# Performance work log

Hardware: AMD Instinct MI355X
Metric: run time of the kernel (lower is better)

Reference implementation:

```python
import jax, jax.numpy as jnp
import numpy as np

B, T, I, H, O = 32, 2048, 512, 512, 256


def setup_inputs() -> dict:
    key = jax.random.key(0)
    ks = jax.random.split(key, 11)
    s_in = 1.0 / np.sqrt(I)  # torch Linear default init bound
    s_h = 1.0 / np.sqrt(H)

    def lin(k, shape, s):
        return jax.random.uniform(k, shape, jnp.float32, -s, s)

    return {
        "x": jax.random.normal(ks[0], (B, T, I), jnp.float32),
        "W_i": lin(ks[1], (H, I), s_in), "b_i": lin(ks[2], (H,), s_in),
        "W_f": lin(ks[3], (H, I), s_in), "b_f": lin(ks[4], (H,), s_in),
        "W_g": lin(ks[5], (H, I), s_in), "b_g": lin(ks[6], (H,), s_in),
        "W_o": lin(ks[7], (H, I), s_in), "b_o": lin(ks[8], (H,), s_in),
        "W_fc": lin(ks[9], (O, H), s_h), "b_fc": lin(ks[10], (O,), s_h),
    }


def reference(x, W_i, b_i, W_f, b_f, W_g, b_g, W_o, b_o, W_fc, b_fc):
    # NOTE: this module's gates depend on x only (not h), so all four gate
    # projections can be precomputed as one pass of GEMMs over [B,T,I].
    gi = jax.nn.sigmoid(jnp.einsum("bti,hi->bth", x, W_i) + b_i)
    gf = jax.nn.sigmoid(jnp.einsum("bti,hi->bth", x, W_f) + b_f)
    gg = jnp.tanh(jnp.einsum("bti,hi->bth", x, W_g) + b_g)
    go = jax.nn.sigmoid(jnp.einsum("bti,hi->bth", x, W_o) + b_o)

    # Sequential elementwise recurrence over time (time-major for scan).
    def step(carry, gates_t):
        _, c = carry
        i, f, g, o = gates_t
        c = f * c + i * g
        h = o * jnp.tanh(c)
        return (h, c), None

    init = (jnp.zeros((B, H), x.dtype), jnp.zeros((B, H), x.dtype))
    gates_tm = (gi.swapaxes(0, 1), gf.swapaxes(0, 1),
                gg.swapaxes(0, 1), go.swapaxes(0, 1))  # each [T,B,H]
    (h, _), _ = jax.lax.scan(step, init, gates_tm)

    return h @ W_fc.T + b_fc  # [B, O]
```

## Files before the change

kernel.cpp:

```cpp
#include <hip/hip_runtime.h>
#include <stdint.h>

#define DI 512
#define DH 512
#define DOUT 256
#define NB 32
#define NT 2048
#define MTOT (NB*NT)
#define NCHUNK 16
#define CLEN 128
#define BM 128
#define BN 64
#define BK 32

typedef unsigned short u16;
typedef __attribute__((ext_vector_type(8))) short bf16x8;
typedef __attribute__((ext_vector_type(4))) short s16x4;
typedef __attribute__((ext_vector_type(4))) float f32x4;

__device__ __forceinline__ u16 f2bf(float f) {
    union { float f; unsigned int u; } c; c.f = f;
    unsigned int u = c.u;
    u += 0x7fffu + ((u >> 16) & 1u);
    return (u16)(u >> 16);
}
__device__ __forceinline__ float bf2f(u16 h) {
    union { unsigned int u; float f; } c; c.u = ((unsigned int)h) << 16;
    return c.f;
}
__device__ __forceinline__ float sigm(float x) { return 1.0f / (1.0f + __expf(-x)); }
__device__ __forceinline__ float tanh_(float x) { return 1.0f - 2.0f / (__expf(2.0f * x) + 1.0f); }

__global__ __launch_bounds__(256)
void cvt_all(const float* __restrict__ X, const float* __restrict__ w0,
             const float* __restrict__ w1, const float* __restrict__ w2,
             u16* __restrict__ xbf, u16* __restrict__ wbf) {
    const int NX4 = MTOT * DI / 4;
    const int NW4 = DH * DI / 4;
    const int total = NX4 + 3 * NW4;
    const int stride = gridDim.x * blockDim.x;
    for (int i = blockIdx.x * blockDim.x + threadIdx.x; i < total; i += stride) {
        const float4* s4; ushort4* d4; int j;
        if (i < NX4) {
            s4 = reinterpret_cast<const float4*>(X);
            d4 = reinterpret_cast<ushort4*>(xbf);
            j = i;
        } else {
            const int k = i - NX4;
            const int w = k >> 16;
            j = k & 65535;
            s4 = reinterpret_cast<const float4*>(w == 0 ? w0 : w == 1 ? w1 : w2);
            d4 = reinterpret_cast<ushort4*>(wbf + (size_t)w * DH * DI);
        }
        float4 v = s4[j];
        unsigned int lo, hi;
        asm("v_cvt_pk_bf16_f32 %0, %1, %2" : "=v"(lo) : "v"(v.x), "v"(v.y));
        asm("v_cvt_pk_bf16_f32 %0, %1, %2" : "=v"(hi) : "v"(v.z), "v"(v.w));
        ushort4 o;
        o.x = (u16)(lo & 0xffffu); o.y = (u16)(lo >> 16);
        o.z = (u16)(hi & 0xffffu); o.w = (u16)(hi >> 16);
        d4[j] = o;
    }
}

__global__ __launch_bounds__(256, 3)
void gate_gemm_scan(const u16* __restrict__ Xbf, const u16* __restrict__ W,
                    const float* __restrict__ b_i, const float* __restrict__ b_f,
                    const float* __restrict__ b_g,
                    float* __restrict__ Ach, float* __restrict__ Vch) {
    __shared__ __align__(16) union {
        struct { u16 sA[2][BM * BK]; u16 sB[2][3 * BN * BK]; } st;
        struct { u16 Ft[BN][132]; u16 Pt[BN][132]; float pa[256]; float pv[256]; } sc;
    } u;

    const int bid0 = blockIdx.x;
    const int swz = (bid0 & 7) * 512 + (bid0 >> 3);
    const int mtile = swz >> 3;
    const int ntile = swz & 7;
    const int m0 = mtile * BM;
    const int n0 = ntile * BN;

    const int tid = threadIdx.x;
    const int lane = tid & 63;
    const int ws = __builtin_amdgcn_readfirstlane(tid >> 6);
    const int wr = ws >> 1;
    const int wc = ws & 1;

    const int srow = lane >> 2;
    const int slot = lane & 3;
    const int fr = lane & 15;
    const int khalf = lane >> 4;

    const int rlA = ws * 32 + srow;
    const int swzslot = slot ^ ((rlA >> 1) & 3);
    const u16* pA0 = Xbf + (size_t)(m0 + rlA) * DI + swzslot * 8;
    const u16* pA1 = pA0 + (size_t)16 * DI;

    const int idx0 = ws * 3;
    const int g0 = idx0 >> 2, cc0 = idx0 & 3;
    const int rlB0 = cc0 * 16 + srow;
    const u16* gaB0 = W + (size_t)g0 * DH * DI + (size_t)(n0 + rlB0) * DI
                    + ((slot ^ ((rlB0 >> 1) & 3)) * 8);
    int dB[3];
    dB[0] = 0;
#pragma unroll
    for (int q = 1; q < 3; ++q) {
        const int idxq = idx0 + q;
        const int gq = idxq >> 2, ccq = idxq & 3;
        dB[q] = __builtin_amdgcn_readfirstlane((gq - g0) * (DH * DI) + (ccq - cc0) * 16 * DI);
    }

    const int rA = wr * 64 + fr;
    const int offA0 = rA * BK + ((khalf ^ ((rA >> 1) & 3)) * 8);
    const int rB = wc * 32 + fr;
    const int offB0 = rB * BK + ((khalf ^ ((rB >> 1) & 3)) * 8);

#define STAGE_A(CB, KT) do {                                                        \
    u16* sAb = u.st.sA[(CB)];                                                       \
    __builtin_amdgcn_global_load_lds(                                               \
        (const __attribute__((address_space(1))) unsigned int*)(pA0 + (KT) * BK),   \
        (__attribute__((address_space(3))) unsigned int*)(sAb + (ws * 2 + 0) * 512),\
        16, 0, 0);                                                                  \
    __builtin_amdgcn_global_load_lds(                                               \
        (const __attribute__((address_space(1))) unsigned int*)(pA1 + (KT) * BK),   \
        (__attribute__((address_space(3))) unsigned int*)(sAb + (ws * 2 + 1) * 512),\
        16, 0, 0);                                                                  \
} while (0)

#define STAGE_B(CB, KT) do {                                                        \
    u16* sBb = u.st.sB[(CB)];                                                       \
    _Pragma("unroll")                                                               \
    for (int q = 0; q < 3; ++q) {                                                   \
        const int idxq = ws * 3 + q;                                                \
        __builtin_amdgcn_global_load_lds(                                           \
            (const __attribute__((address_space(1))) unsigned int*)(gaB0 + dB[q] + (KT) * BK), \
            (__attribute__((address_space(3))) unsigned int*)(sBb + (idxq >> 2) * (BN * BK) + (idxq & 3) * 512), \
            16, 0, 0);                                                              \
    }                                                                               \
} while (0)

    f32x4 acc[3][4][2] = {};

    STAGE_A(0, 0);
    STAGE_B(0, 0);

#define KSTEP(KT) do {                                                              \
    constexpr int cur_ = (KT) & 1;                                                  \
    constexpr int nxt_ = cur_ ^ 1;                                                  \
    if ((KT) < 15) {                                                                \
        STAGE_A(nxt_, (KT) + 1);                                                    \
        STAGE_B(nxt_, (KT) + 1);                                                    \
        asm volatile("s_waitcnt vmcnt(5)" ::: "memory");                            \
    } else {                                                                        \
        asm volatile("s_waitcnt vmcnt(0)" ::: "memory");                            \
    }                                                                               \
    __builtin_amdgcn_sched_barrier(0);                                              \
    __builtin_amdgcn_s_barrier();                                                   \
    {                                                                               \
        const u16* sAb = u.st.sA[cur_];                                             \
        const u16* sBb = u.st.sB[cur_];                                             \
        bf16x8 af[4];                                                               \
        _Pragma("unroll")                                                           \
        for (int m = 0; m < 4; m++)                                                 \
            af[m] = *reinterpret_cast<const bf16x8*>(sAb + offA0 + m * 16 * BK);    \
        __builtin_amdgcn_s_setprio(1);                                              \
        _Pragma("unroll")                                                           \
        for (int g = 0; g < 3; g++) {                                               \
            const u16* sbg = sBb + g * (BN * BK);                                   \
            bf16x8 b0 = *reinterpret_cast<const bf16x8*>(sbg + offB0);              \
            bf16x8 b1 = *reinterpret_cast<const bf16x8*>(sbg + offB0 + 16 * BK);    \
            _Pragma("unroll")                                                       \
            for (int m = 0; m < 4; m++) {                                           \
                acc[g][m][0] = __builtin_amdgcn_mfma_f32_16x16x32_bf16(af[m], b0, acc[g][m][0], 0, 0, 0); \
                acc[g][m][1] = __builtin_amdgcn_mfma_f32_16x16x32_bf16(af[m], b1, acc[g][m][1], 0, 0, 0); \
            }                                                                       \
        }                                                                           \
        __builtin_amdgcn_s_setprio(0);                                              \
    }                                                                               \
    if ((KT) < 15) {                                                                \
        __builtin_amdgcn_sched_barrier(0);                                          \
        __builtin_amdgcn_s_barrier();                                               \
    }                                                                               \
} while (0)

    KSTEP(0);  KSTEP(1);  KSTEP(2);  KSTEP(3);
    KSTEP(4);  KSTEP(5);  KSTEP(6);  KSTEP(7);
    KSTEP(8);  KSTEP(9);  KSTEP(10); KSTEP(11);
    KSTEP(12); KSTEP(13); KSTEP(14); KSTEP(15);
#undef KSTEP
#undef STAGE_B
#undef STAGE_A

    __syncthreads();

    const int rbase = (lane >> 4) * 4;
#pragma unroll
    for (int n = 0; n < 2; n++) {
        const int cl = wc * 32 + n * 16 + fr;
        const int hg = n0 + cl;
        const float bi_ = b_i[hg];
        const float bfv = b_f[hg];
        const float bg_ = b_g[hg];
#pragma unroll
        for (int m = 0; m < 4; m++) {
            const int rr0 = wr * 64 + m * 16 + rbase;
            s16x4 fpk, ppk;
#pragma unroll
            for (int jj = 0; jj < 4; jj++) {
                const float fi = sigm(acc[0][m][n][jj] + bi_);
                const float ff = sigm(acc[1][m][n][jj] + bfv);
                const float fg = tanh_(acc[2][m][n][jj] + bg_);
                fpk[jj] = (short)f2bf(ff);
                ppk[jj] = (short)f2bf(fi * fg);
            }
            *reinterpret_cast<s16x4*>(&u.sc.Ft[cl][rr0]) = fpk;
            *reinterpret_cast<s16x4*>(&u.sc.Pt[cl][rr0]) = ppk;
        }
    }
    __syncthreads();

    {
        const int h = tid & 63;
        const int q = tid >> 6;
        const int t0 = q * 32;
        float a = 1.0f, v = 0.0f;
#pragma unroll
        for (int kk = 0; kk < 8; kk++) {
            s16x4 fv = *reinterpret_cast<const s16x4*>(&u.sc.Ft[h][t0 + kk * 4]);
            s16x4 pv4 = *reinterpret_cast<const s16x4*>(&u.sc.Pt[h][t0 + kk * 4]);
#pragma unroll
            for (int e = 0; e < 4; e++) {
                const float f = bf2f((u16)fv[e]);
                const float p = bf2f((u16)pv4[e]);
                v = f * v + p;
                a *= f;
            }
        }
        u.sc.pa[tid] = a;
        u.sc.pv[tid] = v;
    }
    __syncthreads();

    if (tid < 64) {
        float Aacc = u.sc.pa[tid];
        float Vacc = u.sc.pv[tid];
#pragma unroll
        for (int q = 1; q < 4; q++) {
            const float aq = u.sc.pa[q * 64 + tid];
            const float vq = u.sc.pv[q * 64 + tid];
            Vacc = aq * Vacc + vq;
            Aacc *= aq;
        }
        const size_t o = (size_t)mtile * DH + n0 + tid;
        Ach[o] = Aacc;
        Vch[o] = Vacc;
    }
}

__global__ void cvt_w3(const float* __restrict__ w0, const float* __restrict__ w1,
                       const float* __restrict__ w2, u16* __restrict__ out) {
    const int per = DH * DI / 4;
    int gid = blockIdx.x * blockDim.x + threadIdx.x;
    int wsel = gid / per;
    int i = gid - wsel * per;
    const float* src = (wsel == 0) ? w0 : (wsel == 1) ? w1 : w2;
    float4 v = reinterpret_cast<const float4*>(src)[i];
    ushort4 o;
    o.x = f2bf(v.x); o.y = f2bf(v.y); o.z = f2bf(v.z); o.w = f2bf(v.w);
    reinterpret_cast<ushort4*>(out + (size_t)wsel * DH * DI)[i] = o;
}

__global__ __launch_bounds__(256, 2)
void gate_gemm_scan_fused(const float* __restrict__ X, const u16* __restrict__ W,
                          const float* __restrict__ b_i, const float* __restrict__ b_f,
                          const float* __restrict__ b_g,
                          float* __restrict__ Ach, float* __restrict__ Vch) {
    __shared__ __align__(16) union {
        struct { u16 sA[2][BM * BK]; u16 sB[2][3 * BN * BK]; } st;
        struct { u16 Ft[BN][132]; u16 Pt[BN][132]; float pa[256]; float pv[256]; } sc;
    } u;

    const int bid0 = blockIdx.x;
    const int swz = (bid0 & 7) * 512 + (bid0 >> 3);
    const int mtile = swz >> 3;
    const int ntile = swz & 7;
    const int m0 = mtile * BM;
    const int n0 = ntile * BN;

    const int tid = threadIdx.x;
    const int lane = tid & 63;
    const int ws = __builtin_amdgcn_readfirstlane(tid >> 6);
    const int wr = ws >> 1;
    const int wc = ws & 1;

    const int srow = lane >> 2;
    const int slot = lane & 3;
    const int fr = lane & 15;
    const int khalf = lane >> 4;

    const int rlA = ws * 32 + srow;
    const int swzslot = slot ^ ((rlA >> 1) & 3);
    const float* pXA = X + (size_t)(m0 + rlA) * DI + swzslot * 8;

    const int idx0 = ws * 3;
    const int g0 = idx0 >> 2, cc0 = idx0 & 3;
    const int rlB0 = cc0 * 16 + srow;
    const u16* gaB0 = W + (size_t)g0 * DH * DI + (size_t)(n0 + rlB0) * DI
                    + ((slot ^ ((rlB0 >> 1) & 3)) * 8);
    int dB[3];
    dB[0] = 0;
#pragma unroll
    for (int q = 1; q < 3; ++q) {
        const int idxq = idx0 + q;
        const int gq = idxq >> 2, ccq = idxq & 3;
        dB[q] = __builtin_amdgcn_readfirstlane((gq - g0) * (DH * DI) + (ccq - cc0) * 16 * DI);
    }

    const int rA = wr * 64 + fr;
    const int offA0 = rA * BK + ((khalf ^ ((rA >> 1) & 3)) * 8);
    const int rB = wc * 32 + fr;
    const int offB0 = rB * BK + ((khalf ^ ((rB >> 1) & 3)) * 8);

    float4 fa[2][2][2];

#define LOAD_A(P, KT) do {                                                          \
    _Pragma("unroll")                                                               \
    for (int s = 0; s < 2; ++s) {                                                   \
        fa[(P)][s][0] = *reinterpret_cast<const float4*>(pXA + (size_t)s * 16 * DI + (KT) * 32);     \
        fa[(P)][s][1] = *reinterpret_cast<const float4*>(pXA + (size_t)s * 16 * DI + (KT) * 32 + 4); \
    }                                                                               \
} while (0)

#define CVT_STAGE(P, CB) do {                                                       \
    _Pragma("unroll")                                                               \
    for (int s = 0; s < 2; ++s) {                                                   \
        unsigned int pk0, pk1, pk2, pk3;                                            \
        asm("v_cvt_pk_bf16_f32 %0, %1, %2" : "=v"(pk0) : "v"(fa[(P)][s][0].x), "v"(fa[(P)][s][0].y)); \
        asm("v_cvt_pk_bf16_f32 %0, %1, %2" : "=v"(pk1) : "v"(fa[(P)][s][0].z), "v"(fa[(P)][s][0].w)); \
        asm("v_cvt_pk_bf16_f32 %0, %1, %2" : "=v"(pk2) : "v"(fa[(P)][s][1].x), "v"(fa[(P)][s][1].y)); \
        asm("v_cvt_pk_bf16_f32 %0, %1, %2" : "=v"(pk3) : "v"(fa[(P)][s][1].z), "v"(fa[(P)][s][1].w)); \
        uint4 wv; wv.x = pk0; wv.y = pk1; wv.z = pk2; wv.w = pk3;                   \
        *reinterpret_cast<uint4*>(u.st.sA[(CB)] + ((ws * 2 + s) * 512 + lane * 8)) = wv; \
    }                                                                               \
} while (0)

#define STAGE_B(CB, KT) do {                                                        \
    u16* sBb = u.st.sB[(CB)];                                                       \
    _Pragma("unroll")                                                               \
    for (int q = 0; q < 3; ++q) {                                                   \
        const int idxq = ws * 3 + q;                                                \
        __builtin_amdgcn_global_load_lds(                                           \
            (const __attribute__((address_space(1))) unsigned int*)(gaB0 + dB[q] + (KT) * BK), \
            (__attribute__((address_space(3))) unsigned int*)(sBb + (idxq >> 2) * (BN * BK) + (idxq & 3) * 512), \
            16, 0, 0);                                                              \
    }                                                                               \
} while (0)

    f32x4 acc[3][4][2] = {};

    LOAD_A(0, 0);
    LOAD_A(1, 1);
    CVT_STAGE(0, 0);
    STAGE_B(0, 0);
    asm volatile("s_waitcnt vmcnt(0)" ::: "memory");
    asm volatile("s_waitcnt lgkmcnt(0)" ::: "memory");
    __builtin_amdgcn_sched_barrier(0);
    __builtin_amdgcn_s_barrier();

#define KSTEP(KT) do {                                                              \
    constexpr int cur_ = (KT) & 1;                                                  \
    constexpr int nxt_ = cur_ ^ 1;                                                  \
    if ((KT) < 15) {                                                                \
        CVT_STAGE(nxt_, nxt_);                                                      \
        STAGE_B(nxt_, (KT) + 1);                                                    \
    }                                                                               \
    if ((KT) < 14) LOAD_A(cur_, (KT) + 2);                                          \
    if ((KT) == 15) asm volatile("s_waitcnt vmcnt(0)" ::: "memory");                \
    __builtin_amdgcn_sched_barrier(0);                                              \
    __builtin_amdgcn_s_barrier();                                                   \
    {                                                                               \
        const u16* sAb = u.st.sA[cur_];                                             \
        const u16* sBb = u.st.sB[cur_];                                             \
        bf16x8 af[4];                                                               \
        _Pragma("unroll")                                                           \
        for (int m = 0; m < 4; m++)                                                 \
            af[m] = *reinterpret_cast<const bf16x8*>(sAb + offA0 + m * 16 * BK);    \
        __builtin_amdgcn_s_setprio(1);                                              \
        _Pragma("unroll")                                                           \
        for (int g = 0; g < 3; g++) {                                               \
            const u16* sbg = sBb + g * (BN * BK);                                   \
            bf16x8 b0 = *reinterpret_cast<const bf16x8*>(sbg + offB0);              \
            bf16x8 b1 = *reinterpret_cast<const bf16x8*>(sbg + offB0 + 16 * BK);    \
            _Pragma("unroll")                                                       \
            for (int m = 0; m < 4; m++) {                                           \
                acc[g][m][0] = __builtin_amdgcn_mfma_f32_16x16x32_bf16(af[m], b0, acc[g][m][0], 0, 0, 0); \
                acc[g][m][1] = __builtin_amdgcn_mfma_f32_16x16x32_bf16(af[m], b1, acc[g][m][1], 0, 0, 0); \
            }                                                                       \
        }                                                                           \
        __builtin_amdgcn_s_setprio(0);                                              \
    }                                                                               \
    if ((KT) < 15) {                                                                \
        asm volatile("s_waitcnt lgkmcnt(0)" ::: "memory");                          \
        __builtin_amdgcn_sched_barrier(0);                                          \
        __builtin_amdgcn_s_barrier();                                               \
    }                                                                               \
} while (0)

    KSTEP(0);  KSTEP(1);  KSTEP(2);  KSTEP(3);
    KSTEP(4);  KSTEP(5);  KSTEP(6);  KSTEP(7);
    KSTEP(8);  KSTEP(9);  KSTEP(10); KSTEP(11);
    KSTEP(12); KSTEP(13); KSTEP(14); KSTEP(15);
#undef KSTEP
#undef STAGE_B
#undef CVT_STAGE
#undef LOAD_A

    __syncthreads();

    const int rbase = (lane >> 4) * 4;
#pragma unroll
    for (int n = 0; n < 2; n++) {
        const int cl = wc * 32 + n * 16 + fr;
        const int hg = n0 + cl;
        const float bi_ = b_i[hg];
        const float bfv = b_f[hg];
        const float bg_ = b_g[hg];
#pragma unroll
        for (int m = 0; m < 4; m++) {
            const int rr0 = wr * 64 + m * 16 + rbase;
            s16x4 fpk, ppk;
#pragma unroll
            for (int jj = 0; jj < 4; jj++) {
                const float fi = sigm(acc[0][m][n][jj] + bi_);
                const float ff = sigm(acc[1][m][n][jj] + bfv);
                const float fg = tanh_(acc[2][m][n][jj] + bg_);
                fpk[jj] = (short)f2bf(ff);
                ppk[jj] = (short)f2bf(fi * fg);
            }
            *reinterpret_cast<s16x4*>(&u.sc.Ft[cl][rr0]) = fpk;
            *reinterpret_cast<s16x4*>(&u.sc.Pt[cl][rr0]) = ppk;
        }
    }
    __syncthreads();

    {
        const int h = tid & 63;
        const int q = tid >> 6;
        const int t0 = q * 32;
        float a = 1.0f, v = 0.0f;
#pragma unroll
        for (int kk = 0; kk < 8; kk++) {
            s16x4 fv = *reinterpret_cast<const s16x4*>(&u.sc.Ft[h][t0 + kk * 4]);
            s16x4 pv4 = *reinterpret_cast<const s16x4*>(&u.sc.Pt[h][t0 + kk * 4]);
#pragma unroll
            for (int e = 0; e < 4; e++) {
                const float f = bf2f((u16)fv[e]);
                const float p = bf2f((u16)pv4[e]);
                v = f * v + p;
                a *= f;
            }
        }
        u.sc.pa[tid] = a;
        u.sc.pv[tid] = v;
    }
    __syncthreads();

    if (tid < 64) {
        float Aacc = u.sc.pa[tid];
        float Vacc = u.sc.pv[tid];
#pragma unroll
        for (int q = 1; q < 4; q++) {
            const float aq = u.sc.pa[q * 64 + tid];
            const float vq = u.sc.pv[q * 64 + tid];
            Vacc = aq * Vacc + vq;
            Aacc *= aq;
        }
        const size_t o = (size_t)mtile * DH + n0 + tid;
        Ach[o] = Aacc;
        Vch[o] = Vacc;
    }
}

__global__ __launch_bounds__(512)
void finalize_fc(const float* __restrict__ Ach, const float* __restrict__ Vch,
                 const float* __restrict__ x, const float* __restrict__ Wo,
                 const float* __restrict__ bo, const float* __restrict__ Wfc,
                 const float* __restrict__ bfc, float* __restrict__ out) {
    __shared__ float xrow[DI];
    __shared__ float hrow[DH];
    const int b = blockIdx.x;
    const int tid = threadIdx.x;

    xrow[tid] = x[((size_t)b * NT + (NT - 1)) * DI + tid];
    float c = 0.0f;
#pragma unroll
    for (int jj = 0; jj < NCHUNK; jj++) {
        const size_t o = ((size_t)(b * NCHUNK + jj)) * DH + tid;
        c = Ach[o] * c + Vch[o];
    }
    __syncthreads();

    {
        const float4* xr = reinterpret_cast<const float4*>(xrow);
        const float4* wrow = reinterpret_cast<const float4*>(Wo + (size_t)tid * DI);
        float dot = 0.0f;
#pragma unroll 4
        for (int k = 0; k < DI / 4; k++) {
            float4 xv = xr[k];
            float4 wv = wrow[k];
            dot += xv.x * wv.x + xv.y * wv.y + xv.z * wv.z + xv.w * wv.w;
        }
        const float og = sigm(dot + bo[tid]);
        hrow[tid] = og * tanh_(c);
    }
    __syncthreads();

    if (tid < DOUT) {
        const float4* hr = reinterpret_cast<const float4*>(hrow);
        const float4* wrow = reinterpret_cast<const float4*>(Wfc + (size_t)tid * DH);
        float acc = 0.0f;
#pragma unroll 4
        for (int k = 0; k < DH / 4; k++) {
            float4 hv = hr[k];
            float4 wv = wrow[k];
            acc += hv.x * wv.x + hv.y * wv.y + hv.z * wv.z + hv.w * wv.w;
        }
        out[b * DOUT + tid] = acc + bfc[tid];
    }
}

extern "C" void kernel_launch(void* const* d_in, const int* in_sizes, int n_in,
                              void* d_out, int out_size, void* d_ws, size_t ws_size,
                              hipStream_t stream) {
    const float* x    = (const float*)d_in[0];
    const float* W_i  = (const float*)d_in[1];
    const float* b_i  = (const float*)d_in[2];
    const float* W_f  = (const float*)d_in[3];
    const float* b_f  = (const float*)d_in[4];
    const float* W_g  = (const float*)d_in[5];
    const float* b_g  = (const float*)d_in[6];
    const float* W_o  = (const float*)d_in[7];
    const float* b_o  = (const float*)d_in[8];
    const float* W_fc = (const float*)d_in[9];
    const float* b_fc = (const float*)d_in[10];
    float* out = (float*)d_out;

    char* ws = (char*)d_ws;
    const size_t XBF_BYTES = (size_t)MTOT * DI * 2;
    const size_t WBF_BYTES = (size_t)3 * DH * DI * 2;
    const size_t AV_BYTES  = (size_t)MTOT / CLEN * DH * 4;
    const size_t NEED = XBF_BYTES + WBF_BYTES + 2 * AV_BYTES;

    if (ws_size >= NEED) {
        u16* xbf   = (u16*)ws;
        u16* wbf   = (u16*)(ws + XBF_BYTES);
        float* Ach = (float*)(ws + XBF_BYTES + WBF_BYTES);
        float* Vch = (float*)(ws + XBF_BYTES + WBF_BYTES + AV_BYTES);

        cvt_all<<<4096, 256, 0, stream>>>(x, W_i, W_f, W_g, xbf, wbf);
        gate_gemm_scan<<<4096, 256, 0, stream>>>(xbf, wbf, b_i, b_f, b_g, Ach, Vch);
        finalize_fc<<<32, 512, 0, stream>>>(Ach, Vch, x, W_o, b_o, W_fc, b_fc, out);
    } else {
        u16* wbf    = (u16*)ws;
        float* Ach  = (float*)(ws + 1572864);
        float* Vch  = (float*)(ws + 2621440);

        cvt_w3<<<768, 256, 0, stream>>>(W_i, W_f, W_g, wbf);
        gate_gemm_scan_fused<<<4096, 256, 0, stream>>>(x, wbf, b_i, b_f, b_g, Ach, Vch);
        finalize_fc<<<32, 512, 0, stream>>>(Ach, Vch, x, W_o, b_o, W_fc, b_fc, out);
    }
}
```

Measured before the change: 199.4 us.

## Double GEMM M-tile to 256 rows and widen conversion stores to 16 bytes

```diff
diff --git a/kernel.cpp b/kernel.cpp
--- a/kernel.cpp
+++ b/kernel.cpp
@@ -10,6 +10,7 @@
 #define NCHUNK 16
 #define CLEN 128
 #define BM 128
+#define BM2 256
 #define BN 64
 #define BK 32
 
@@ -35,49 +36,50 @@
 void cvt_all(const float* __restrict__ X, const float* __restrict__ w0,
              const float* __restrict__ w1, const float* __restrict__ w2,
              u16* __restrict__ xbf, u16* __restrict__ wbf) {
-    const int NX4 = MTOT * DI / 4;
-    const int NW4 = DH * DI / 4;
-    const int total = NX4 + 3 * NW4;
+    const int NX8 = MTOT * DI / 8;
+    const int NW8 = DH * DI / 8;
+    const int total = NX8 + 3 * NW8;
     const int stride = gridDim.x * blockDim.x;
     for (int i = blockIdx.x * blockDim.x + threadIdx.x; i < total; i += stride) {
-        const float4* s4; ushort4* d4; int j;
-        if (i < NX4) {
+        const float4* s4; uint4* d4; int j;
+        if (i < NX8) {
             s4 = reinterpret_cast<const float4*>(X);
-            d4 = reinterpret_cast<ushort4*>(xbf);
+            d4 = reinterpret_cast<uint4*>(xbf);
             j = i;
         } else {
-            const int k = i - NX4;
-            const int w = k >> 16;
-            j = k & 65535;
+            const int k = i - NX8;
+            const int w = k >> 15;
+            j = k & (NW8 - 1);
             s4 = reinterpret_cast<const float4*>(w == 0 ? w0 : w == 1 ? w1 : w2);
-            d4 = reinterpret_cast<ushort4*>(wbf + (size_t)w * DH * DI);
-        }
-        float4 v = s4[j];
-        unsigned int lo, hi;
-        asm("v_cvt_pk_bf16_f32 %0, %1, %2" : "=v"(lo) : "v"(v.x), "v"(v.y));
-        asm("v_cvt_pk_bf16_f32 %0, %1, %2" : "=v"(hi) : "v"(v.z), "v"(v.w));
-        ushort4 o;
-        o.x = (u16)(lo & 0xffffu); o.y = (u16)(lo >> 16);
-        o.z = (u16)(hi & 0xffffu); o.w = (u16)(hi >> 16);
+            d4 = reinterpret_cast<uint4*>(wbf + (size_t)w * DH * DI);
+        }
+        float4 v0 = s4[2 * j];
+        float4 v1 = s4[2 * j + 1];
+        unsigned int p0, p1, p2, p3;
+        asm("v_cvt_pk_bf16_f32 %0, %1, %2" : "=v"(p0) : "v"(v0.x), "v"(v0.y));
+        asm("v_cvt_pk_bf16_f32 %0, %1, %2" : "=v"(p1) : "v"(v0.z), "v"(v0.w));
+        asm("v_cvt_pk_bf16_f32 %0, %1, %2" : "=v"(p2) : "v"(v1.x), "v"(v1.y));
+        asm("v_cvt_pk_bf16_f32 %0, %1, %2" : "=v"(p3) : "v"(v1.z), "v"(v1.w));
+        uint4 o; o.x = p0; o.y = p1; o.z = p2; o.w = p3;
         d4[j] = o;
     }
 }
 
-__global__ __launch_bounds__(256, 3)
+__global__ __launch_bounds__(256, 2)
 void gate_gemm_scan(const u16* __restrict__ Xbf, const u16* __restrict__ W,
                     const float* __restrict__ b_i, const float* __restrict__ b_f,
                     const float* __restrict__ b_g,
                     float* __restrict__ Ach, float* __restrict__ Vch) {
     __shared__ __align__(16) union {
-        struct { u16 sA[2][BM * BK]; u16 sB[2][3 * BN * BK]; } st;
-        struct { u16 Ft[BN][132]; u16 Pt[BN][132]; float pa[256]; float pv[256]; } sc;
+        struct { u16 sA[2][BM2 * BK]; u16 sB[2][3 * BN * BK]; } st;
+        struct { u16 Ft[BN][260]; u16 Pt[BN][260]; float pa[256]; float pv[256]; } sc;
     } u;
 
     const int bid0 = blockIdx.x;
-    const int swz = (bid0 & 7) * 512 + (bid0 >> 3);
-    const int mtile = swz >> 3;
+    const int swz = (bid0 & 7) * 256 + (bid0 >> 3);
+    const int mtp = swz >> 3;
     const int ntile = swz & 7;
-    const int m0 = mtile * BM;
+    const int m0 = mtp * BM2;
     const int n0 = ntile * BN;
 
     const int tid = threadIdx.x;
@@ -91,10 +93,9 @@
     const int fr = lane & 15;
     const int khalf = lane >> 4;
 
-    const int rlA = ws * 32 + srow;
-    const int swzslot = slot ^ ((rlA >> 1) & 3);
-    const u16* pA0 = Xbf + (size_t)(m0 + rlA) * DI + swzslot * 8;
-    const u16* pA1 = pA0 + (size_t)16 * DI;
+    const int rlA = ws * 64 + srow;
+    const int swzslotA = slot ^ ((srow >> 1) & 3);
+    const u16* pA = Xbf + (size_t)(m0 + rlA) * DI + swzslotA * 8;
 
     const int idx0 = ws * 3;
     const int g0 = idx0 >> 2, cc0 = idx0 & 3;
@@ -110,21 +111,20 @@
         dB[q] = __builtin_amdgcn_readfirstlane((gq - g0) * (DH * DI) + (ccq - cc0) * 16 * DI);
     }
 
-    const int rA = wr * 64 + fr;
+    const int rA = wr * 128 + fr;
     const int offA0 = rA * BK + ((khalf ^ ((rA >> 1) & 3)) * 8);
     const int rB = wc * 32 + fr;
     const int offB0 = rB * BK + ((khalf ^ ((rB >> 1) & 3)) * 8);
 
 #define STAGE_A(CB, KT) do {                                                        \
     u16* sAb = u.st.sA[(CB)];                                                       \
-    __builtin_amdgcn_global_load_lds(                                               \
-        (const __attribute__((address_space(1))) unsigned int*)(pA0 + (KT) * BK),   \
-        (__attribute__((address_space(3))) unsigned int*)(sAb + (ws * 2 + 0) * 512),\
-        16, 0, 0);                                                                  \
-    __builtin_amdgcn_global_load_lds(                                               \
-        (const __attribute__((address_space(1))) unsigned int*)(pA1 + (KT) * BK),   \
-        (__attribute__((address_space(3))) unsigned int*)(sAb + (ws * 2 + 1) * 512),\
-        16, 0, 0);                                                                  \
+    _Pragma("unroll")                                                               \
+    for (int j = 0; j < 4; ++j) {                                                   \
+        __builtin_amdgcn_global_load_lds(                                           \
+            (const __attribute__((address_space(1))) unsigned int*)(pA + (size_t)j * 16 * DI + (KT) * BK), \
+            (__attribute__((address_space(3))) unsigned int*)(sAb + (ws * 4 + j) * 512), \
+            16, 0, 0);                                                              \
+    }                                                                               \
 } while (0)
 
 #define STAGE_B(CB, KT) do {                                                        \
@@ -139,7 +139,7 @@
     }                                                                               \
 } while (0)
 
-    f32x4 acc[3][4][2] = {};
+    f32x4 acc[3][8][2] = {};
 
     STAGE_A(0, 0);
     STAGE_B(0, 0);
@@ -150,7 +150,7 @@
     if ((KT) < 15) {                                                                \
         STAGE_A(nxt_, (KT) + 1);                                                    \
         STAGE_B(nxt_, (KT) + 1);                                                    \
-        asm volatile("s_waitcnt vmcnt(5)" ::: "memory");                            \
+        asm volatile("s_waitcnt vmcnt(7)" ::: "memory");                            \
     } else {                                                                        \
         asm volatile("s_waitcnt vmcnt(0)" ::: "memory");                            \
     }                                                                               \
@@ -159,20 +159,27 @@
     {                                                                               \
         const u16* sAb = u.st.sA[cur_];                                             \
         const u16* sBb = u.st.sB[cur_];                                             \
-        bf16x8 af[4];                                                               \
-        _Pragma("unroll")                                                           \
-        for (int m = 0; m < 4; m++)                                                 \
-            af[m] = *reinterpret_cast<const bf16x8*>(sAb + offA0 + m * 16 * BK);    \
-        __builtin_amdgcn_s_setprio(1);                                              \
+        bf16x8 bfr[3][2];                                                           \
         _Pragma("unroll")                                                           \
         for (int g = 0; g < 3; g++) {                                               \
             const u16* sbg = sBb + g * (BN * BK);                                   \
-            bf16x8 b0 = *reinterpret_cast<const bf16x8*>(sbg + offB0);              \
-            bf16x8 b1 = *reinterpret_cast<const bf16x8*>(sbg + offB0 + 16 * BK);    \
+            bfr[g][0] = *reinterpret_cast<const bf16x8*>(sbg + offB0);              \
+            bfr[g][1] = *reinterpret_cast<const bf16x8*>(sbg + offB0 + 16 * BK);    \
+        }                                                                           \
+        __builtin_amdgcn_s_setprio(1);                                              \
+        _Pragma("unroll")                                                           \
+        for (int mh = 0; mh < 2; mh++) {                                            \
+            bf16x8 af[4];                                                           \
+            _Pragma("unroll")                                                       \
+            for (int m = 0; m < 4; m++)                                             \
+                af[m] = *reinterpret_cast<const bf16x8*>(sAb + offA0 + (mh * 4 + m) * 16 * BK); \
             _Pragma("unroll")                                                       \
             for (int m = 0; m < 4; m++) {                                           \
-                acc[g][m][0] = __builtin_amdgcn_mfma_f32_16x16x32_bf16(af[m], b0, acc[g][m][0], 0, 0, 0); \
-                acc[g][m][1] = __builtin_amdgcn_mfma_f32_16x16x32_bf16(af[m], b1, acc[g][m][1], 0, 0, 0); \
+                _Pragma("unroll")                                                   \
+                for (int g = 0; g < 3; g++) {                                       \
+                    acc[g][mh * 4 + m][0] = __builtin_amdgcn_mfma_f32_16x16x32_bf16(af[m], bfr[g][0], acc[g][mh * 4 + m][0], 0, 0, 0); \
+                    acc[g][mh * 4 + m][1] = __builtin_amdgcn_mfma_f32_16x16x32_bf16(af[m], bfr[g][1], acc[g][mh * 4 + m][1], 0, 0, 0); \
+                }                                                                   \
             }                                                                       \
         }                                                                           \
         __builtin_amdgcn_s_setprio(0);                                              \
@@ -202,8 +209,8 @@
         const float bfv = b_f[hg];
         const float bg_ = b_g[hg];
 #pragma unroll
-        for (int m = 0; m < 4; m++) {
-            const int rr0 = wr * 64 + m * 16 + rbase;
+        for (int m = 0; m < 8; m++) {
+            const int rr0 = wr * 128 + m * 16 + rbase;
             s16x4 fpk, ppk;
 #pragma unroll
             for (int jj = 0; jj < 4; jj++) {
@@ -221,11 +228,11 @@
 
     {
         const int h = tid & 63;
-        const int q = tid >> 6;
-        const int t0 = q * 32;
+        const int seg = tid >> 6;
+        const int t0 = seg * 64;
         float a = 1.0f, v = 0.0f;
 #pragma unroll
-        for (int kk = 0; kk < 8; kk++) {
+        for (int kk = 0; kk < 16; kk++) {
             s16x4 fv = *reinterpret_cast<const s16x4*>(&u.sc.Ft[h][t0 + kk * 4]);
             s16x4 pv4 = *reinterpret_cast<const s16x4*>(&u.sc.Pt[h][t0 + kk * 4]);
 #pragma unroll
@@ -241,17 +248,16 @@
     }
     __syncthreads();
 
-    if (tid < 64) {
-        float Aacc = u.sc.pa[tid];
-        float Vacc = u.sc.pv[tid];
-#pragma unroll
-        for (int q = 1; q < 4; q++) {
-            const float aq = u.sc.pa[q * 64 + tid];
-            const float vq = u.sc.pv[q * 64 + tid];
-            Vacc = aq * Vacc + vq;
-            Aacc *= aq;
-        }
-        const size_t o = (size_t)mtile * DH + n0 + tid;
+    if (tid < 128) {
+        const int c = tid >> 6;
+        const int h = tid & 63;
+        float Aacc = u.sc.pa[c * 128 + h];
+        float Vacc = u.sc.pv[c * 128 + h];
+        const float aq = u.sc.pa[c * 128 + 64 + h];
+        const float vq = u.sc.pv[c * 128 + 64 + h];
+        Vacc = aq * Vacc + vq;
+        Aacc *= aq;
+        const size_t o = (size_t)(2 * mtp + c) * DH + n0 + h;
         Ach[o] = Aacc;
         Vch[o] = Vacc;
     }
@@ -557,8 +563,8 @@
         float* Ach = (float*)(ws + XBF_BYTES + WBF_BYTES);
         float* Vch = (float*)(ws + XBF_BYTES + WBF_BYTES + AV_BYTES);
 
-        cvt_all<<<4096, 256, 0, stream>>>(x, W_i, W_f, W_g, xbf, wbf);
-        gate_gemm_scan<<<4096, 256, 0, stream>>>(xbf, wbf, b_i, b_f, b_g, Ach, Vch);
+        cvt_all<<<2048, 256, 0, stream>>>(x, W_i, W_f, W_g, xbf, wbf);
+        gate_gemm_scan<<<2048, 256, 0, stream>>>(xbf, wbf, b_i, b_f, b_g, Ach, Vch);
         finalize_fc<<<32, 512, 0, stream>>>(Ach, Vch, x, W_o, b_o, W_fc, b_fc, out);
     } else {
         u16* wbf    = (u16*)ws;
```

New measurement: 207.2 us. 1.04x slower.
